# Performance work log

Measured on AMD Instinct MI355X. Metric: run time of the kernel, lower is better.

The kernel has to match this reference:

```python
import jax, jax.numpy as jnp
import numpy as np

N, E, IN, H, OUT, G = 100000, 1600000, 9, 64, 6, 1024
EPS = 1e-5


def setup_inputs() -> dict:
    key = jax.random.key(0)
    ks = jax.random.split(key, 24)
    inp = {
        "x": jax.random.normal(ks[0], (N, IN), dtype=jnp.float32),
        "edge_index": jax.random.randint(ks[1], (2, E), 0, N, dtype=jnp.int64),
        "edge_weight": jax.random.uniform(ks[2], (E,), dtype=jnp.float32),
        "batch": jnp.sort(jax.random.randint(ks[3], (N,), 0, G, dtype=jnp.int64)),
    }
    def lin(k, fan_in, fan_out):
        return jax.random.normal(k, (fan_in, fan_out), dtype=jnp.float32) / np.sqrt(fan_in)
    # GraphConv layer 0: IN -> H; layers 1,2: H -> H
    inp["W_rel0"], inp["W_root0"], inp["b0"] = lin(ks[4], IN, H), lin(ks[5], IN, H), jnp.zeros((H,), jnp.float32)
    inp["W_rel1"], inp["W_root1"], inp["b1"] = lin(ks[6], H, H), lin(ks[7], H, H), jnp.zeros((H,), jnp.float32)
    inp["W_rel2"], inp["W_root2"], inp["b2"] = lin(ks[8], H, H), lin(ks[9], H, H), jnp.zeros((H,), jnp.float32)
    # BatchNorm params for the first num_layers-1 = 2 layers
    inp["g0"], inp["be0"] = jnp.ones((H,), jnp.float32), jnp.zeros((H,), jnp.float32)
    inp["g1"], inp["be1"] = jnp.ones((H,), jnp.float32), jnp.zeros((H,), jnp.float32)
    # MLP head
    inp["W_l1"], inp["b_l1"] = lin(ks[10], H, H), jnp.zeros((H,), jnp.float32)
    inp["W_l2"], inp["b_l2"] = lin(ks[11], H, OUT), jnp.zeros((OUT,), jnp.float32)
    return inp


def graph_conv(x, src, dst, ew, W_rel, W_root, b):
    # PyG GraphConv: out = aggr_add(e_ji * x_j) @ W_rel + b + x @ W_root
    msg = x[src] * ew[:, None]                      # [E, F] gather
    agg = jax.ops.segment_sum(msg, dst, num_segments=x.shape[0])  # [N, F] scatter-add
    return agg @ W_rel + b + x @ W_root


def batch_norm(x, g, b):
    m = jnp.mean(x, axis=0)
    v = jnp.var(x, axis=0)
    return (x - m) * jax.lax.rsqrt(v + EPS) * g + b


def reference(x, edge_index, edge_weight, batch,
              W_rel0, W_root0, b0, W_rel1, W_root1, b1, W_rel2, W_root2, b2,
              g0, be0, g1, be1, W_l1, b_l1, W_l2, b_l2):
    src, dst = edge_index[0], edge_index[1]
    # layer 0: conv -> BN -> relu (dropout p applied only in training; eval here)
    h = graph_conv(x, src, dst, edge_weight, W_rel0, W_root0, b0)
    h = jax.nn.relu(batch_norm(h, g0, be0))
    # layer 1
    h = graph_conv(h, src, dst, edge_weight, W_rel1, W_root1, b1)
    h = jax.nn.relu(batch_norm(h, g1, be1))
    # layer 2 (no norm/relu)
    h = graph_conv(h, src, dst, edge_weight, W_rel2, W_root2, b2)
    # global mean pool over graphs
    summed = jax.ops.segment_sum(h, batch, num_segments=G)            # [G, H]
    counts = jax.ops.segment_sum(jnp.ones((h.shape[0],), h.dtype), batch, num_segments=G)
    pooled = summed / jnp.maximum(counts, 1.0)[:, None]
    # MLP head
    z = jax.nn.relu(pooled @ W_l1 + b_l1)
    return z @ W_l2 + b_l2
```

## Files before the change

kernel.cpp:

```cpp
#include <hip/hip_runtime.h>
#include <hip/hip_fp16.h>

constexpr int N    = 100000;
constexpr int E    = 1600000;
constexpr int FIN  = 9;
constexpr int OUTF = 6;
constexpr int G    = 1024;
constexpr int NPB  = 256;
constexpr int NB   = (N + NPB - 1) / NPB;
constexpr int CH   = 2048;
constexpr int NCH  = (E + CH - 1) / CH;
constexpr int BCAP = 4864;
constexpr int CBCAP= BCAP + NPB + 8;
constexpr int EBUF = 5888;
constexpr int ZCNT = 256 + G * 64;

typedef _Float16 f16x8 __attribute__((ext_vector_type(8)));
typedef float    f32x4 __attribute__((ext_vector_type(4)));

__device__ __forceinline__ void atomAddF(float* p, float v) { unsafeAtomicAdd(p, v); }

__device__ __forceinline__ float us2f(unsigned short u) {
    return __half2float(__builtin_bit_cast(__half, u));
}

__global__ __launch_bounds__(256) void initK(int* __restrict__ cursor, float* __restrict__ zeros,
    const float* __restrict__ x, __half* __restrict__ x9)
{
    int i = blockIdx.x * 256 + threadIdx.x;
    if (i < NB) cursor[i] = i * BCAP;
    if (i < ZCNT) zeros[i] = 0.f;
    if (i < N * FIN) x9[i] = __float2half(x[i]);
}

__global__ __launch_bounds__(256) void passA(const int* __restrict__ src, const int* __restrict__ dst,
    const float* __restrict__ ew, int* __restrict__ cursor, int2* __restrict__ bucketed)
{
    __shared__ int h[NB];
    __shared__ int hb[NB];
    int t = threadIdx.x;
    for (int i = t; i < NB; i += 256) h[i] = 0;
    __syncthreads();
    int base = blockIdx.x * CH;
    int myS[8], myD[8], rk[8]; float myW[8];
#pragma unroll
    for (int i = 0; i < 8; i++) {
        int e = base + i * 256 + t;
        if (e < E) {
            myS[i] = src[e]; myD[i] = dst[e]; myW[i] = ew[e];
            rk[i] = atomicAdd(&h[myD[i] >> 8], 1);
        } else myD[i] = -1;
    }
    __syncthreads();
    for (int i = t; i < NB; i += 256) hb[i] = h[i] ? atomicAdd(&cursor[i], h[i]) : 0;
    __syncthreads();
#pragma unroll
    for (int i = 0; i < 8; i++) if (myD[i] >= 0) {
        int packed = myS[i] | ((myD[i] & 255) << 24);
        bucketed[hb[myD[i] >> 8] + rk[i]] = make_int2(packed, __float_as_int(myW[i]));
    }
}

__global__ __launch_bounds__(NPB) void passB(const int* __restrict__ cursor,
    const int2* __restrict__ bucketed, int* __restrict__ ebeg, int* __restrict__ eend,
    int2* __restrict__ csr)
{
    __shared__ int2 ebuf[EBUF];
    __shared__ int cl[NPB], sa[NPB], sb[NPB], curs[NPB];
    int b = blockIdx.x, t = threadIdx.x;
    int node0 = b * NPB;
    int nnode = min(NPB, N - node0);
    int cnt = cursor[b] - b * BCAP;
    int abase = b * BCAP;
    int base = b * CBCAP;
    bool fits = (cnt <= EBUF);
    cl[t] = 0;
    __syncthreads();
    for (int e = t; e < cnt; e += NPB) {
        int2 r = bucketed[abase + e];
        if (fits) ebuf[e] = r;
        atomicAdd(&cl[((unsigned)r.x) >> 24], 1);
    }
    __syncthreads();
    int deg = cl[t];
    int pc = (deg + 1) & ~1;
    int* cur = sa; int* nxt = sb;
    cur[t] = pc;
    __syncthreads();
    for (int o = 1; o < NPB; o <<= 1) {
        int v = cur[t];
        if (t >= o) v += cur[t - o];
        nxt[t] = v;
        __syncthreads();
        int* tmp = cur; cur = nxt; nxt = tmp;
    }
    int off = cur[t] - pc;
    if (t < nnode) { ebeg[node0 + t] = base + off; eend[node0 + t] = base + off + deg; }
    curs[t] = off;
    __syncthreads();
    for (int e = t; e < cnt; e += NPB) {
        int2 r = fits ? ebuf[e] : bucketed[abase + e];
        int dl = ((unsigned)r.x) >> 24;
        int pos = base + atomicAdd(&curs[dl], 1);
        csr[pos] = make_int2(r.x & 0x00FFFFFF, r.y);
    }
    __syncthreads();
    if (t < nnode && (deg & 1)) csr[base + off + deg] = make_int2(0, 0);
    if (t < 4) csr[base + cur[NPB - 1] + t] = make_int2(0, 0);
}

__global__ __launch_bounds__(256) void wprep(const float* __restrict__ Wrel1, const float* __restrict__ Wroot1,
    const float* __restrict__ Wrel2, const float* __restrict__ Wroot2, __half* __restrict__ Wt)
{
    int i = blockIdx.x * 256 + threadIdx.x;
    int layer = i >> 13, r = i & 8191;
    int c = r >> 6, k = r & 63;
    const float* Wrel = layer ? Wrel2 : Wrel1;
    const float* Wroot = layer ? Wroot2 : Wroot1;
    float v = (c < 64) ? Wrel[k * 64 + c] : Wroot[k * 64 + (c - 64)];
    Wt[i] = __float2half(v);
}

__global__ __launch_bounds__(256, 2) void gather9(const __half* __restrict__ x9h,
    const int2* __restrict__ csr, const int* __restrict__ ebeg, const int* __restrict__ eend,
    float* __restrict__ agg9)
{
    const unsigned short* __restrict__ x9 = (const unsigned short*)x9h;
    int t = threadIdx.x, lane = t & 63;
    int es = lane >> 4, fc = min(lane & 15, FIN - 1);
    int wv = __builtin_amdgcn_readfirstlane((blockIdx.x * blockDim.x + t) >> 6);
    int nw = (gridDim.x * blockDim.x) >> 6;
    for (int n = wv; n < N; n += nw) {
        int beg = ebeg[n], end = eend[n];
        int last = end - 1;
        int2 eA0 = csr[min(beg + es,      last)];
        int2 eB0 = csr[min(beg + 4 + es,  last)];
        int2 eA1 = csr[min(beg + 8 + es,  last)];
        int2 eB1 = csr[min(beg + 12 + es, last)];
        unsigned short xA = x9[(size_t)eA0.x * FIN + fc];
        unsigned short xB = x9[(size_t)eB0.x * FIN + fc];
        float a0 = 0.f, a1 = 0.f;
        for (int k = beg; k < end; k += 8) {
            int2 eA2 = csr[min(k + 16 + es, last)];
            int2 eB2 = csr[min(k + 20 + es, last)];
            unsigned short nxA = x9[(size_t)eA1.x * FIN + fc];
            unsigned short nxB = x9[(size_t)eB1.x * FIN + fc];
            float wA = (k + es     < end) ? __int_as_float(eA0.y) : 0.f;
            float wB = (k + 4 + es < end) ? __int_as_float(eB0.y) : 0.f;
            a0 = fmaf(wA, us2f(xA), a0);
            a1 = fmaf(wB, us2f(xB), a1);
            eA0 = eA1; eB0 = eB1; eA1 = eA2; eB1 = eB2;
            xA = nxA; xB = nxB;
        }
        float r = a0 + a1;
        r += __shfl(r, lane ^ 16, 64);
        r += __shfl(r, lane ^ 32, 64);
        if (lane < FIN) agg9[(size_t)n * FIN + lane] = r;
    }
}

__global__ __launch_bounds__(256) void proj0post(const float* __restrict__ x,
    const float* __restrict__ agg9, const float* __restrict__ Wrel,
    const float* __restrict__ Wroot, const float* __restrict__ bias,
    __half* __restrict__ H0, float* __restrict__ stats)
{
    int t = threadIdx.x, j = t & 63;
    int nl = __builtin_amdgcn_readfirstlane(t >> 6);
    float wrel[FIN], wroot[FIN];
#pragma unroll
    for (int k = 0; k < FIN; k++) { wrel[k] = Wrel[k * 64 + j]; wroot[k] = Wroot[k * 64 + j]; }
    float bj = bias[j];
    float s1 = 0.f, s2 = 0.f;
    const int ntiles = N / 4;
    for (int tile = blockIdx.x; tile < ntiles; tile += gridDim.x) {
        int n = tile * 4 + nl;
        const float* xr = x + (size_t)n * FIN;
        const float* ar = agg9 + (size_t)n * FIN;
        float acc = bj;
#pragma unroll
        for (int k = 0; k < FIN; k++) {
            acc = fmaf(ar[k], wrel[k], acc);
            acc = fmaf(xr[k], wroot[k], acc);
        }
        H0[(size_t)n * 64 + j] = __float2half(acc);
        s1 += acc; s2 += acc * acc;
    }
    __shared__ float sred[256];
    sred[t] = s1; __syncthreads();
    if (t < 64) atomAddF(&stats[t], sred[t] + sred[t+64] + sred[t+128] + sred[t+192]);
    __syncthreads();
    sred[t] = s2; __syncthreads();
    if (t < 64) atomAddF(&stats[64 + t], sred[t] + sred[t+64] + sred[t+128] + sred[t+192]);
}

__global__ __launch_bounds__(256) void projm(const __half* __restrict__ Hin, const __half* __restrict__ Wt,
    const float* __restrict__ bias, const float* __restrict__ stats,
    const float* __restrict__ gam, const float* __restrict__ bet,
    __half* __restrict__ P, __half* __restrict__ Hout)
{
    int t = threadIdx.x, lane = t & 63;
    int wv = blockIdx.x * 4 + (t >> 6);
    int nw = gridDim.x * 4;
    int n16 = lane & 15, quad = lane >> 4;
    constexpr float invN = 1.0f / (float)N;
    float sc[16], sh[16];
#pragma unroll
    for (int jj = 0; jj < 16; jj++) {
        int k = (jj < 8) ? (quad * 8 + jj) : (32 + quad * 8 + (jj - 8));
        float m = stats[k] * invN;
        float v = stats[64 + k] * invN - m * m;
        sc[jj] = gam[k] * rsqrtf(v + 1e-5f);
        sh[jj] = bet[k] - m * sc[jj];
    }
    f16x8 bf[8][2];
#pragma unroll
    for (int ct = 0; ct < 8; ct++)
#pragma unroll
        for (int kh = 0; kh < 2; kh++)
            bf[ct][kh] = *(const f16x8*)(Wt + (size_t)(ct * 16 + n16) * 64 + kh * 32 + quad * 8);
    float bcol[4];
#pragma unroll
    for (int i = 0; i < 4; i++) bcol[i] = bias[i * 16 + n16];
    const int NT = N / 16;
    for (int tile = wv; tile < NT; tile += nw) {
        int n0 = tile * 16;
        f16x8 r0 = *(const f16x8*)(Hin + (size_t)(n0 + n16) * 64 + quad * 8);
        f16x8 r1 = *(const f16x8*)(Hin + (size_t)(n0 + n16) * 64 + 32 + quad * 8);
        f16x8 a0, a1;
#pragma unroll
        for (int jj = 0; jj < 8; jj++) {
            a0[jj] = (_Float16)fmaxf(fmaf((float)r0[jj], sc[jj],     sh[jj]),     0.f);
            a1[jj] = (_Float16)fmaxf(fmaf((float)r1[jj], sc[jj + 8], sh[jj + 8]), 0.f);
        }
        f32x4 acc[8];
#pragma unroll
        for (int ct = 0; ct < 8; ct++) {
            f32x4 c = {0.f, 0.f, 0.f, 0.f};
            c = __builtin_amdgcn_mfma_f32_16x16x32_f16(a0, bf[ct][0], c, 0, 0, 0);
            c = __builtin_amdgcn_mfma_f32_16x16x32_f16(a1, bf[ct][1], c, 0, 0, 0);
            acc[ct] = c;
        }
#pragma unroll
        for (int ct = 0; ct < 8; ct++) {
#pragma unroll
            for (int r = 0; r < 4; r++) {
                int n = n0 + quad * 4 + r;
                if (ct < 4) P[(size_t)n * 64 + ct * 16 + n16] = __float2half(acc[ct][r]);
                else Hout[(size_t)n * 64 + (ct - 4) * 16 + n16] = __float2half(acc[ct][r] + bcol[ct - 4]);
            }
        }
    }
}

template<int EPI>
__global__ __launch_bounds__(256, 2) void gather(const __half* __restrict__ Ph, __half* H,
    const int2* __restrict__ csr, const int* __restrict__ ebeg, const int* __restrict__ eend,
    float* __restrict__ stats, const int* __restrict__ batch, float* __restrict__ pool)
{
    const unsigned short* __restrict__ P = (const unsigned short*)Ph;
    int t = threadIdx.x, lane = t & 63;
    int wv = __builtin_amdgcn_readfirstlane((blockIdx.x * blockDim.x + t) >> 6);
    int nw = (gridDim.x * blockDim.x) >> 6;
    float s1 = 0.f, s2 = 0.f;
    const int NQ = N / 4;
    for (int g = wv; g < NQ; g += nw) {
        int n0 = 4 * g;
        int b0 = ebeg[n0],     m0 = (eend[n0]     - b0 + 1) >> 1;
        int b1 = ebeg[n0 + 1], m1 = (eend[n0 + 1] - b1 + 1) >> 1;
        int b2 = ebeg[n0 + 2], m2 = (eend[n0 + 2] - b2 + 1) >> 1;
        int b3 = ebeg[n0 + 3], m3 = (eend[n0 + 3] - b3 + 1) >> 1;
        const int4* q0 = (const int4*)csr + (b0 >> 1);
        const int4* q1 = (const int4*)csr + (b1 >> 1);
        const int4* q2 = (const int4*)csr + (b2 >> 1);
        const int4* q3 = (const int4*)csr + (b3 >> 1);
        int c0 = max(m0 - 1, 0), c1 = max(m1 - 1, 0);
        int c2 = max(m2 - 1, 0), c3 = max(m3 - 1, 0);
        float x0 = __half2float(H[(size_t)(n0    ) * 64 + lane]);
        float x1 = __half2float(H[(size_t)(n0 + 1) * 64 + lane]);
        float x2 = __half2float(H[(size_t)(n0 + 2) * 64 + lane]);
        float x3 = __half2float(H[(size_t)(n0 + 3) * 64 + lane]);
        float a00 = 0.f, a01 = 0.f, a02 = 0.f, a03 = 0.f;
        float a10 = 0.f, a11 = 0.f, a12 = 0.f, a13 = 0.f;
        float a20 = 0.f, a21 = 0.f, a22 = 0.f, a23 = 0.f;
        float a30 = 0.f, a31 = 0.f, a32 = 0.f, a33 = 0.f;
        int mm = max(max(m0, m1), max(m2, m3));
        for (int k = 0; k < mm; k += 2) {
            int4 pA0 = q0[min(k, c0)], pB0 = q0[min(k + 1, c0)];
            int4 pA1 = q1[min(k, c1)], pB1 = q1[min(k + 1, c1)];
            int4 pA2 = q2[min(k, c2)], pB2 = q2[min(k + 1, c2)];
            int4 pA3 = q3[min(k, c3)], pB3 = q3[min(k + 1, c3)];
            unsigned short rA00 = P[(size_t)pA0.x * 64 + lane], rA01 = P[(size_t)pA0.z * 64 + lane];
            unsigned short rB00 = P[(size_t)pB0.x * 64 + lane], rB01 = P[(size_t)pB0.z * 64 + lane];
            unsigned short rA10 = P[(size_t)pA1.x * 64 + lane], rA11 = P[(size_t)pA1.z * 64 + lane];
            unsigned short rB10 = P[(size_t)pB1.x * 64 + lane], rB11 = P[(size_t)pB1.z * 64 + lane];
            unsigned short rA20 = P[(size_t)pA2.x * 64 + lane], rA21 = P[(size_t)pA2.z * 64 + lane];
            unsigned short rB20 = P[(size_t)pB2.x * 64 + lane], rB21 = P[(size_t)pB2.z * 64 + lane];
            unsigned short rA30 = P[(size_t)pA3.x * 64 + lane], rA31 = P[(size_t)pA3.z * 64 + lane];
            unsigned short rB30 = P[(size_t)pB3.x * 64 + lane], rB31 = P[(size_t)pB3.z * 64 + lane];
            float wA00 = (k < m0) ? __int_as_float(pA0.y) : 0.f;
            float wA01 = (k < m0) ? __int_as_float(pA0.w) : 0.f;
            float wB00 = (k + 1 < m0) ? __int_as_float(pB0.y) : 0.f;
            float wB01 = (k + 1 < m0) ? __int_as_float(pB0.w) : 0.f;
            float wA10 = (k < m1) ? __int_as_float(pA1.y) : 0.f;
            float wA11 = (k < m1) ? __int_as_float(pA1.w) : 0.f;
            float wB10 = (k + 1 < m1) ? __int_as_float(pB1.y) : 0.f;
            float wB11 = (k + 1 < m1) ? __int_as_float(pB1.w) : 0.f;
            float wA20 = (k < m2) ? __int_as_float(pA2.y) : 0.f;
            float wA21 = (k < m2) ? __int_as_float(pA2.w) : 0.f;
            float wB20 = (k + 1 < m2) ? __int_as_float(pB2.y) : 0.f;
            float wB21 = (k + 1 < m2) ? __int_as_float(pB2.w) : 0.f;
            float wA30 = (k < m3) ? __int_as_float(pA3.y) : 0.f;
            float wA31 = (k < m3) ? __int_as_float(pA3.w) : 0.f;
            float wB30 = (k + 1 < m3) ? __int_as_float(pB3.y) : 0.f;
            float wB31 = (k + 1 < m3) ? __int_as_float(pB3.w) : 0.f;
            a00 = fmaf(wA00, us2f(rA00), a00); a01 = fmaf(wA01, us2f(rA01), a01);
            a02 = fmaf(wB00, us2f(rB00), a02); a03 = fmaf(wB01, us2f(rB01), a03);
            a10 = fmaf(wA10, us2f(rA10), a10); a11 = fmaf(wA11, us2f(rA11), a11);
            a12 = fmaf(wB10, us2f(rB10), a12); a13 = fmaf(wB11, us2f(rB11), a13);
            a20 = fmaf(wA20, us2f(rA20), a20); a21 = fmaf(wA21, us2f(rA21), a21);
            a22 = fmaf(wB20, us2f(rB20), a22); a23 = fmaf(wB21, us2f(rB21), a23);
            a30 = fmaf(wA30, us2f(rA30), a30); a31 = fmaf(wA31, us2f(rA31), a31);
            a32 = fmaf(wB30, us2f(rB30), a32); a33 = fmaf(wB31, us2f(rB31), a33);
        }
        float r0 = x0 + ((a00 + a02) + (a01 + a03));
        float r1 = x1 + ((a10 + a12) + (a11 + a13));
        float r2 = x2 + ((a20 + a22) + (a21 + a23));
        float r3 = x3 + ((a30 + a32) + (a31 + a33));
        if constexpr (EPI == 0) {
            H[(size_t)(n0    ) * 64 + lane] = __float2half(r0);
            H[(size_t)(n0 + 1) * 64 + lane] = __float2half(r1);
            H[(size_t)(n0 + 2) * 64 + lane] = __float2half(r2);
            H[(size_t)(n0 + 3) * 64 + lane] = __float2half(r3);
            s1 += (r0 + r1) + (r2 + r3);
            s2 += (r0 * r0 + r1 * r1) + (r2 * r2 + r3 * r3);
        } else {
            atomAddF(&pool[batch[n0    ] * 64 + lane], r0);
            atomAddF(&pool[batch[n0 + 1] * 64 + lane], r1);
            atomAddF(&pool[batch[n0 + 2] * 64 + lane], r2);
            atomAddF(&pool[batch[n0 + 3] * 64 + lane], r3);
        }
    }
    if constexpr (EPI == 0) {
        __shared__ float sred[256];
        sred[t] = s1; __syncthreads();
        if (t < 64) atomAddF(&stats[t], sred[t] + sred[t+64] + sred[t+128] + sred[t+192]);
        __syncthreads();
        sred[t] = s2; __syncthreads();
        if (t < 64) atomAddF(&stats[64 + t], sred[t] + sred[t+64] + sred[t+128] + sred[t+192]);
    }
}

__global__ __launch_bounds__(64) void head(const float* __restrict__ pool,
    const int* __restrict__ batch, const float* __restrict__ Wl1, const float* __restrict__ bl1,
    const float* __restrict__ Wl2, const float* __restrict__ bl2, float* __restrict__ out)
{
    int g = blockIdx.x, t = threadIdx.x;
    __shared__ float sp[64];
    __shared__ float sz[64];
    __shared__ int scnt;
    if (t == 0) {
        int lo = 0, hi = N;
        while (lo < hi) { int m = (lo + hi) >> 1; if (batch[m] < g) lo = m + 1; else hi = m; }
        int lo2 = lo, hi2 = N;
        while (lo2 < hi2) { int m = (lo2 + hi2) >> 1; if (batch[m] < g + 1) lo2 = m + 1; else hi2 = m; }
        scnt = lo2 - lo;
    }
    __syncthreads();
    float cnt = fmaxf((float)scnt, 1.0f);
    sp[t] = pool[g * 64 + t] / cnt;
    __syncthreads();
    float acc = bl1[t];
#pragma unroll
    for (int k = 0; k < 64; k++) acc = fmaf(sp[k], Wl1[k * 64 + t], acc);
    sz[t] = fmaxf(acc, 0.f);
    __syncthreads();
    if (t < OUTF) {
        float o = bl2[t];
#pragma unroll
        for (int k = 0; k < 64; k++) o = fmaf(sz[k], Wl2[k * OUTF + t], o);
        out[g * OUTF + t] = o;
    }
}

extern "C" void kernel_launch(void* const* d_in, const int* in_sizes, int n_in,
                              void* d_out, int out_size, void* d_ws, size_t ws_size,
                              hipStream_t stream)
{
    const float* x     = (const float*)d_in[0];
    const int*   ei    = (const int*)d_in[1];
    const float* ew    = (const float*)d_in[2];
    const int*   batch = (const int*)d_in[3];
    const float* Wrel0 = (const float*)d_in[4];
    const float* Wroot0= (const float*)d_in[5];
    const float* b0    = (const float*)d_in[6];
    const float* Wrel1 = (const float*)d_in[7];
    const float* Wroot1= (const float*)d_in[8];
    const float* b1    = (const float*)d_in[9];
    const float* Wrel2 = (const float*)d_in[10];
    const float* Wroot2= (const float*)d_in[11];
    const float* b2    = (const float*)d_in[12];
    const float* g0    = (const float*)d_in[13];
    const float* be0   = (const float*)d_in[14];
    const float* g1    = (const float*)d_in[15];
    const float* be1   = (const float*)d_in[16];
    const float* Wl1   = (const float*)d_in[17];
    const float* bl1   = (const float*)d_in[18];
    const float* Wl2   = (const float*)d_in[19];
    const float* bl2   = (const float*)d_in[20];
    const int* srcI = ei;
    const int* dstI = ei + E;

    __half* Ha     = (__half*)d_ws;
    __half* Hb     = Ha + (size_t)N * 64;
    __half* P      = Hb + (size_t)N * 64;
    int2*   csr    = (int2*)(P + (size_t)N * 64);
    int*    ebeg   = (int*)(csr + (size_t)NB * CBCAP);
    int*    eend   = ebeg + N;
    int*    cursor = eend + N;
    float*  stats0 = (float*)(cursor + NB);
    float*  stats1 = stats0 + 128;
    float*  pool   = stats1 + 128;
    __half* Wt1    = (__half*)(pool + G * 64);
    __half* Wt2    = Wt1 + 128 * 64;
    float*  agg9   = (float*)(Wt2 + 128 * 64);
    __half* x9     = (__half*)(agg9 + (size_t)N * FIN);
    int2*   bucketed = (int2*)Ha;

    initK<<<(N * FIN + 255) / 256, 256, 0, stream>>>(cursor, stats0, x, x9);
    passA<<<NCH, 256, 0, stream>>>(srcI, dstI, ew, cursor, bucketed);
    passB<<<NB, NPB, 0, stream>>>(cursor, bucketed, ebeg, eend, csr);
    wprep<<<64, 256, 0, stream>>>(Wrel1, Wroot1, Wrel2, Wroot2, Wt1);

    gather9<<<2048, 256, 0, stream>>>(x9, csr, ebeg, eend, agg9);
    proj0post<<<2048, 256, 0, stream>>>(x, agg9, Wrel0, Wroot0, b0, Ha, stats0);

    projm<<<1024, 256, 0, stream>>>(Ha, Wt1, b1, stats0, g0, be0, P, Hb);
    gather<0><<<2048, 256, 0, stream>>>(P, Hb, csr, ebeg, eend, stats1, nullptr, nullptr);

    projm<<<1024, 256, 0, stream>>>(Hb, Wt2, b2, stats1, g1, be1, P, Ha);
    gather<1><<<2048, 256, 0, stream>>>(P, Ha, csr, ebeg, eend, nullptr, batch, pool);

    head<<<G, 64, 0, stream>>>(pool, batch, Wl1, bl1, Wl2, bl2, (float*)d_out);
}
```

Before: 444.5 us.

## Fuse layer-0 projection into gather9, pad x9 to 16, use nontemporal loads/stores

Merges the layer-0 projection and BN statistics kernel into the gather kernel, using wave shuffles to broadcast the aggregated features. This drops one launch and the agg9 round trip through memory. The fp16 copy of x is padded to 16 features per row so gather reads are aligned. H buffers are now read and written with nontemporal loads and stores, which may lower cache pollution but could hurt if those rows were reused from cache.

```diff
diff --git a/kernel.cpp b/kernel.cpp
--- a/kernel.cpp
+++ b/kernel.cpp
@@ -23,6 +23,15 @@
 __device__ __forceinline__ float us2f(unsigned short u) {
     return __half2float(__builtin_bit_cast(__half, u));
 }
+__device__ __forceinline__ unsigned short ntld_us(const unsigned short* p) {
+    return __builtin_nontemporal_load(p);
+}
+__device__ __forceinline__ void ntst_us(unsigned short* p, unsigned short v) {
+    __builtin_nontemporal_store(v, p);
+}
+__device__ __forceinline__ unsigned short h2us(float f) {
+    return __builtin_bit_cast(unsigned short, __float2half(f));
+}
 
 __global__ __launch_bounds__(256) void initK(int* __restrict__ cursor, float* __restrict__ zeros,
     const float* __restrict__ x, __half* __restrict__ x9)
@@ -30,7 +39,10 @@
     int i = blockIdx.x * 256 + threadIdx.x;
     if (i < NB) cursor[i] = i * BCAP;
     if (i < ZCNT) zeros[i] = 0.f;
-    if (i < N * FIN) x9[i] = __float2half(x[i]);
+    if (i < N * 16) {
+        int n = i >> 4, f = i & 15;
+        x9[i] = __float2half(f < FIN ? x[n * FIN + f] : 0.f);
+    }
 }
 
 __global__ __launch_bounds__(256) void passA(const int* __restrict__ src, const int* __restrict__ dst,
@@ -123,11 +135,17 @@
 
 __global__ __launch_bounds__(256, 2) void gather9(const __half* __restrict__ x9h,
     const int2* __restrict__ csr, const int* __restrict__ ebeg, const int* __restrict__ eend,
-    float* __restrict__ agg9)
+    const float* __restrict__ x, const float* __restrict__ Wrel, const float* __restrict__ Wroot,
+    const float* __restrict__ bias, __half* __restrict__ H0, float* __restrict__ stats)
 {
     const unsigned short* __restrict__ x9 = (const unsigned short*)x9h;
     int t = threadIdx.x, lane = t & 63;
-    int es = lane >> 4, fc = min(lane & 15, FIN - 1);
+    int es = lane >> 4, fc = lane & 15;
+    float wrel[FIN], wroot[FIN];
+#pragma unroll
+    for (int k = 0; k < FIN; k++) { wrel[k] = Wrel[k * 64 + lane]; wroot[k] = Wroot[k * 64 + lane]; }
+    float bj = bias[lane];
+    float s1 = 0.f, s2 = 0.f;
     int wv = __builtin_amdgcn_readfirstlane((blockIdx.x * blockDim.x + t) >> 6);
     int nw = (gridDim.x * blockDim.x) >> 6;
     for (int n = wv; n < N; n += nw) {
@@ -137,14 +155,14 @@
         int2 eB0 = csr[min(beg + 4 + es,  last)];
         int2 eA1 = csr[min(beg + 8 + es,  last)];
         int2 eB1 = csr[min(beg + 12 + es, last)];
-        unsigned short xA = x9[(size_t)eA0.x * FIN + fc];
-        unsigned short xB = x9[(size_t)eB0.x * FIN + fc];
+        unsigned short xA = x9[(size_t)eA0.x * 16 + fc];
+        unsigned short xB = x9[(size_t)eB0.x * 16 + fc];
         float a0 = 0.f, a1 = 0.f;
         for (int k = beg; k < end; k += 8) {
             int2 eA2 = csr[min(k + 16 + es, last)];
             int2 eB2 = csr[min(k + 20 + es, last)];
-            unsigned short nxA = x9[(size_t)eA1.x * FIN + fc];
-            unsigned short nxB = x9[(size_t)eB1.x * FIN + fc];
+            unsigned short nxA = x9[(size_t)eA1.x * 16 + fc];
+            unsigned short nxB = x9[(size_t)eB1.x * 16 + fc];
             float wA = (k + es     < end) ? __int_as_float(eA0.y) : 0.f;
             float wB = (k + 4 + es < end) ? __int_as_float(eB0.y) : 0.f;
             a0 = fmaf(wA, us2f(xA), a0);
@@ -155,34 +173,16 @@
         float r = a0 + a1;
         r += __shfl(r, lane ^ 16, 64);
         r += __shfl(r, lane ^ 32, 64);
-        if (lane < FIN) agg9[(size_t)n * FIN + lane] = r;
-    }
-}
-
-__global__ __launch_bounds__(256) void proj0post(const float* __restrict__ x,
-    const float* __restrict__ agg9, const float* __restrict__ Wrel,
-    const float* __restrict__ Wroot, const float* __restrict__ bias,
-    __half* __restrict__ H0, float* __restrict__ stats)
-{
-    int t = threadIdx.x, j = t & 63;
-    int nl = __builtin_amdgcn_readfirstlane(t >> 6);
-    float wrel[FIN], wroot[FIN];
-#pragma unroll
-    for (int k = 0; k < FIN; k++) { wrel[k] = Wrel[k * 64 + j]; wroot[k] = Wroot[k * 64 + j]; }
-    float bj = bias[j];
-    float s1 = 0.f, s2 = 0.f;
-    const int ntiles = N / 4;
-    for (int tile = blockIdx.x; tile < ntiles; tile += gridDim.x) {
-        int n = tile * 4 + nl;
-        const float* xr = x + (size_t)n * FIN;
-        const float* ar = agg9 + (size_t)n * FIN;
+        float xv = (fc < FIN) ? x[(size_t)n * FIN + fc] : 0.f;
         float acc = bj;
 #pragma unroll
-        for (int k = 0; k < FIN; k++) {
-            acc = fmaf(ar[k], wrel[k], acc);
-            acc = fmaf(xr[k], wroot[k], acc);
-        }
-        H0[(size_t)n * 64 + j] = __float2half(acc);
+        for (int f = 0; f < FIN; f++) {
+            float af = __shfl(r,  f, 64);
+            float xf = __shfl(xv, f, 64);
+            acc = fmaf(af, wrel[f], acc);
+            acc = fmaf(xf, wroot[f], acc);
+        }
+        ntst_us((unsigned short*)H0 + (size_t)n * 64 + lane, h2us(acc));
         s1 += acc; s2 += acc * acc;
     }
     __shared__ float sred[256];
@@ -224,8 +224,8 @@
     const int NT = N / 16;
     for (int tile = wv; tile < NT; tile += nw) {
         int n0 = tile * 16;
-        f16x8 r0 = *(const f16x8*)(Hin + (size_t)(n0 + n16) * 64 + quad * 8);
-        f16x8 r1 = *(const f16x8*)(Hin + (size_t)(n0 + n16) * 64 + 32 + quad * 8);
+        f16x8 r0 = __builtin_nontemporal_load((const f16x8*)(Hin + (size_t)(n0 + n16) * 64 + quad * 8));
+        f16x8 r1 = __builtin_nontemporal_load((const f16x8*)(Hin + (size_t)(n0 + n16) * 64 + 32 + quad * 8));
         f16x8 a0, a1;
 #pragma unroll
         for (int jj = 0; jj < 8; jj++) {
@@ -246,7 +246,8 @@
             for (int r = 0; r < 4; r++) {
                 int n = n0 + quad * 4 + r;
                 if (ct < 4) P[(size_t)n * 64 + ct * 16 + n16] = __float2half(acc[ct][r]);
-                else Hout[(size_t)n * 64 + (ct - 4) * 16 + n16] = __float2half(acc[ct][r] + bcol[ct - 4]);
+                else ntst_us((unsigned short*)Hout + (size_t)n * 64 + (ct - 4) * 16 + n16,
+                             h2us(acc[ct][r] + bcol[ct - 4]));
             }
         }
     }
@@ -275,10 +276,10 @@
         const int4* q3 = (const int4*)csr + (b3 >> 1);
         int c0 = max(m0 - 1, 0), c1 = max(m1 - 1, 0);
         int c2 = max(m2 - 1, 0), c3 = max(m3 - 1, 0);
-        float x0 = __half2float(H[(size_t)(n0    ) * 64 + lane]);
-        float x1 = __half2float(H[(size_t)(n0 + 1) * 64 + lane]);
-        float x2 = __half2float(H[(size_t)(n0 + 2) * 64 + lane]);
-        float x3 = __half2float(H[(size_t)(n0 + 3) * 64 + lane]);
+        float x0 = us2f(ntld_us((const unsigned short*)H + (size_t)(n0    ) * 64 + lane));
+        float x1 = us2f(ntld_us((const unsigned short*)H + (size_t)(n0 + 1) * 64 + lane));
+        float x2 = us2f(ntld_us((const unsigned short*)H + (size_t)(n0 + 2) * 64 + lane));
+        float x3 = us2f(ntld_us((const unsigned short*)H + (size_t)(n0 + 3) * 64 + lane));
         float a00 = 0.f, a01 = 0.f, a02 = 0.f, a03 = 0.f;
         float a10 = 0.f, a11 = 0.f, a12 = 0.f, a13 = 0.f;
         float a20 = 0.f, a21 = 0.f, a22 = 0.f, a23 = 0.f;
@@ -327,10 +328,10 @@
         float r2 = x2 + ((a20 + a22) + (a21 + a23));
         float r3 = x3 + ((a30 + a32) + (a31 + a33));
         if constexpr (EPI == 0) {
-            H[(size_t)(n0    ) * 64 + lane] = __float2half(r0);
-            H[(size_t)(n0 + 1) * 64 + lane] = __float2half(r1);
-            H[(size_t)(n0 + 2) * 64 + lane] = __float2half(r2);
-            H[(size_t)(n0 + 3) * 64 + lane] = __float2half(r3);
+            ntst_us((unsigned short*)H + (size_t)(n0    ) * 64 + lane, h2us(r0));
+            ntst_us((unsigned short*)H + (size_t)(n0 + 1) * 64 + lane, h2us(r1));
+            ntst_us((unsigned short*)H + (size_t)(n0 + 2) * 64 + lane, h2us(r2));
+            ntst_us((unsigned short*)H + (size_t)(n0 + 3) * 64 + lane, h2us(r3));
             s1 += (r0 + r1) + (r2 + r3);
             s2 += (r0 * r0 + r1 * r1) + (r2 * r2 + r3 * r3);
         } else {
@@ -422,17 +423,15 @@
     float*  pool   = stats1 + 128;
     __half* Wt1    = (__half*)(pool + G * 64);
     __half* Wt2    = Wt1 + 128 * 64;
-    float*  agg9   = (float*)(Wt2 + 128 * 64);
-    __half* x9     = (__half*)(agg9 + (size_t)N * FIN);
+    __half* x9     = Wt2 + 128 * 64;
     int2*   bucketed = (int2*)Ha;
 
-    initK<<<(N * FIN + 255) / 256, 256, 0, stream>>>(cursor, stats0, x, x9);
+    initK<<<(N * 16 + 255) / 256, 256, 0, stream>>>(cursor, stats0, x, x9);
     passA<<<NCH, 256, 0, stream>>>(srcI, dstI, ew, cursor, bucketed);
     passB<<<NB, NPB, 0, stream>>>(cursor, bucketed, ebeg, eend, csr);
     wprep<<<64, 256, 0, stream>>>(Wrel1, Wroot1, Wrel2, Wroot2, Wt1);
 
-    gather9<<<2048, 256, 0, stream>>>(x9, csr, ebeg, eend, agg9);
-    proj0post<<<2048, 256, 0, stream>>>(x, agg9, Wrel0, Wroot0, b0, Ha, stats0);
+    gather9<<<2048, 256, 0, stream>>>(x9, csr, ebeg, eend, x, Wrel0, Wroot0, b0, Ha, stats0);
 
     projm<<<1024, 256, 0, stream>>>(Ha, Wt1, b1, stats0, g0, be0, P, Hb);
     gather<0><<<2048, 256, 0, stream>>>(P, Hb, csr, ebeg, eend, stats1, nullptr, nullptr);
```

After: 447.6 us. About the same (+0.7%).
